# Performance work log

Hardware: AMD Instinct MI355X
Metric: run time of the kernel (lower is better)

The kernel has to match this reference:

```python
import jax, jax.numpy as jnp
import numpy as np

B, T, I, H, F1, C = 512, 128, 128, 768, 256, 10


def setup_inputs() -> dict:
    key = jax.random.key(0)
    ks = jax.random.split(key, 9)
    s = 1.0 / np.sqrt(H).astype(np.float32)  # torch GRUCell/Linear-style scale
    return {
        "x": jax.random.normal(ks[0], (B, T, I), dtype=jnp.float32),
        "w_ih": jax.random.uniform(ks[1], (3 * H, I), jnp.float32, -s, s),
        "w_hh": jax.random.uniform(ks[2], (3 * H, H), jnp.float32, -s, s),
        "b_ih": jax.random.uniform(ks[3], (3 * H,), jnp.float32, -s, s),
        "b_hh": jax.random.uniform(ks[4], (3 * H,), jnp.float32, -s, s),
        "w_fc1": jax.random.uniform(ks[5], (F1, H), jnp.float32, -s, s),
        "b_fc1": jax.random.uniform(ks[6], (F1,), jnp.float32, -s, s),
        "w_fc2": jax.random.uniform(ks[7], (C, F1), jnp.float32, -s, s),
        "b_fc2": jax.random.uniform(ks[8], (C,), jnp.float32, -s, s),
    }


def reference(x, w_ih, w_hh, b_ih, b_hh, w_fc1, b_fc1, w_fc2, b_fc2):
    # x: [B, T, I]. Input projection for all timesteps in one GEMM (same math
    # as per-step GRUCell, since gi does not depend on h).
    gi = jnp.einsum("bti,gi->btg", x, w_ih) + b_ih  # [B, T, 3H]
    h0 = jnp.zeros((x.shape[0], w_hh.shape[1]), x.dtype)

    def step(h, gi_t):
        gh = h @ w_hh.T + b_hh  # [B, 3H]
        i_r, i_z, i_n = jnp.split(gi_t, 3, axis=-1)
        h_r, h_z, h_n = jnp.split(gh, 3, axis=-1)
        r = jax.nn.sigmoid(i_r + h_r)
        z = jax.nn.sigmoid(i_z + h_z)
        n = jnp.tanh(i_n + r * h_n)
        h_new = (1.0 - z) * n + z * h
        return h_new, None

    h, _ = jax.lax.scan(step, h0, jnp.swapaxes(gi, 0, 1))  # scan over T
    out = jax.nn.relu(h @ w_fc1.T + b_fc1)
    logits = out @ w_fc2.T + b_fc2
    return logits
```

## Files before the change

kernel.cpp:

```cpp
#include <hip/hip_runtime.h>
#include <hip/hip_bf16.h>


typedef unsigned short u16;
typedef float    f32x4    __attribute__((ext_vector_type(4)));
typedef unsigned uint32x4 __attribute__((ext_vector_type(4)));
typedef __bf16   bf16x8   __attribute__((ext_vector_type(8)));

#define MFMA16 __builtin_amdgcn_mfma_f32_16x16x32_bf16

#define GLOAD16(gp, lp)                                                        \
  __builtin_amdgcn_global_load_lds(                                            \
      (const __attribute__((address_space(1))) void*)(gp),                     \
      (__attribute__((address_space(3))) void*)(lp), 16, 0, 0)
#define GLOAD16C(gp, lp)                                                       \
  __builtin_amdgcn_global_load_lds(                                            \
      (const __attribute__((address_space(1))) void*)(gp),                     \
      (__attribute__((address_space(3))) void*)(lp), 16, 0, 1)

__device__ __forceinline__ float bf2f(u16 u) {
  unsigned v = ((unsigned)u) << 16;
  return __builtin_bit_cast(float, v);
}
__device__ __forceinline__ u16 f2bf(float f) {
  unsigned x = __builtin_bit_cast(unsigned, f);
  unsigned r = (x + 0x7fffu + ((x >> 16) & 1u)) >> 16;
  return (u16)r;
}
__device__ __forceinline__ float sigm(float x) {
  x = fminf(fmaxf(x, -30.f), 30.f);
  return 1.f / (1.f + __expf(-x));
}
__device__ __forceinline__ float tanhx(float x) {
  x = fminf(fmaxf(x, -15.f), 15.f);
  float ex = __expf(2.f * x);
  return (ex - 1.f) / (ex + 1.f);
}

__global__ __launch_bounds__(256) void k_prep_w(
    const float* __restrict__ w_ih, const float* __restrict__ w_hh,
    u16* __restrict__ Wg) {
  int idx = blockIdx.x * 256 + threadIdx.x;
  int e = idx & 7, c8 = (idx >> 3) & 7;
  int r3 = idx >> 6;
  int r = r3 % 72;
  int jbt = r3 / 72;
  int bt = jbt % 14, jb = jbt / 14;
  int kc = c8 ^ (r & 7);
  int k = bt * 64 + kc * 8 + e;
  int g = r / 24, c = r % 24;
  int grow = g * 768 + jb * 24 + c;
  float v = (k < 768) ? w_hh[grow * 768 + k] : w_ih[grow * 128 + (k - 768)];
  Wg[idx] = f2bf(v);
}

__global__ __launch_bounds__(256) void k_prep_x(
    const float* __restrict__ x, u16* __restrict__ xpk) {
  int idx = blockIdx.x * 256 + threadIdx.x;
  int e = idx & 7, c16 = (idx >> 3) & 15;
  int row = (idx >> 7) & 511;
  int tb = idx >> 16;
  int bt = tb & 1, t = tb >> 1;
  int lc = c16 ^ (row & 15);
  int hl = lc >> 3, kc = lc & 7;
  int i = bt * 64 + kc * 8 + e;
  float v = x[(row * 128 + t) * 128 + i];
  u16 h = f2bf(v);
  xpk[idx] = hl ? f2bf(v - bf2f(h)) : h;
}

__global__ __launch_bounds__(256) void k_prep_fc1t(
    const float* __restrict__ w_fc1, float* __restrict__ wT) {
  int idx = blockIdx.x * 256 + threadIdx.x;
  int k = idx >> 8, n = idx & 255;
  wT[idx] = w_fc1[n * 768 + k];
}

__global__ __launch_bounds__(512) void k_gru_all(
    const u16* __restrict__ Wg, const u16* __restrict__ xpk,
    u16* __restrict__ hA, u16* __restrict__ hB,
    const float* __restrict__ b_ih, const float* __restrict__ b_hh,
    unsigned* __restrict__ bar, unsigned* __restrict__ ctl) {
  __shared__ __align__(16) u16 sW[64512];
  __shared__ __align__(16) u16 sA[2][8192];
  __shared__ unsigned s_asn;
  const int tid = threadIdx.x;
  const int lane = tid & 63, wv = tid >> 6;
  const int mg = wv & 3, sg = wv >> 2;
  const int l15 = lane & 15, lg = lane >> 4;

  if (tid == 0) {
    unsigned xcd;
    asm volatile("s_getreg_b32 %0, hwreg(HW_REG_XCC_ID, 0, 32)" : "=s"(xcd));
    xcd &= 7u;
    unsigned slot = __hip_atomic_fetch_add(&ctl[xcd * 32], 1u,
        __ATOMIC_RELAXED, __HIP_MEMORY_SCOPE_AGENT);
    __hip_atomic_fetch_add(&ctl[256], 1u, __ATOMIC_RELEASE,
                           __HIP_MEMORY_SCOPE_AGENT);
    while (__hip_atomic_load(&ctl[256], __ATOMIC_RELAXED,
                             __HIP_MEMORY_SCOPE_AGENT) < 256u)
      __builtin_amdgcn_s_sleep(8);
    __builtin_amdgcn_fence(__ATOMIC_ACQUIRE, "agent");
    bool ok = (slot < 32u);
    for (int xx = 0; xx < 8; ++xx)
      ok &= (__hip_atomic_load(&ctl[xx * 32], __ATOMIC_RELAXED,
                               __HIP_MEMORY_SCOPE_AGENT) == 32u);
    unsigned bgv, jbv, fen;
    if (ok) { bgv = xcd; jbv = slot; fen = 0u; }
    else    { bgv = (unsigned)blockIdx.x >> 5;
              jbv = (unsigned)blockIdx.x & 31u; fen = 1u; }
    s_asn = bgv | (jbv << 3) | (fen << 8);
  }
  __syncthreads();
  const unsigned asn = s_asn;
  const int bg = asn & 7, jb = (asn >> 3) & 31;
  const bool fence = (asn >> 8) & 1;
  const int mbase = bg * 64;

  {
    const u16* wbase = Wg + (size_t)jb * 64512;
    for (int ch = wv; ch < 126; ch += 8)
      GLOAD16(wbase + ch * 512 + lane * 8, &sW[ch * 512]);
  }
  asm volatile("s_waitcnt vmcnt(0)" ::: "memory");
  __syncthreads();

  const int cc = sg * 16 + l15;
  const int ccv = (cc < 24) ? cc : (cc - 8);
  int aOff[2][2], bOff[3][2];
#pragma unroll
  for (int kk = 0; kk < 2; ++kk) {
    const int sw = (((kk << 2) + lg) ^ (l15 & 7)) << 3;
#pragma unroll
    for (int hl = 0; hl < 2; ++hl)
      aOff[kk][hl] = (mg * 16 + l15) * 128 +
                     ((((hl << 3) + (kk << 2) + lg) ^ l15) << 3);
#pragma unroll
    for (int g = 0; g < 3; ++g)
      bOff[g][kk] = (g * 24 + ccv) * 64 + sw;
  }
  const int schunk = wv * 2;

  const int j = jb * 24 + cc;
  const bool jvalid = (cc < 24);
  float br = 0.f, bz = 0.f, bni = 0.f, bnh = 0.f;
  if (jvalid) {
    br = b_ih[j] + b_hh[j];
    bz = b_ih[768 + j] + b_hh[768 + j];
    bni = b_ih[1536 + j]; bnh = b_hh[1536 + j];
  }
  const int ebt = j >> 6, ekr = j & 63;
  const int ekc = ekr >> 3, eke = ekr & 7;
  unsigned* mybar = bar + bg * 32;

#pragma unroll 1
  for (int t = 0; t < 128; ++t) {
    const u16* hcur = (t & 1) ? hB : hA;
    u16* hnxt = (t & 1) ? hA : hB;
    const u16* xpt = xpk + (size_t)t * 131072;
    const u16* hsl = hcur + mbase * 128;
    const u16* xsl = xpt + mbase * 128;

    f32x4 acc0 = {0.f, 0.f, 0.f, 0.f};
    f32x4 acc1 = {0.f, 0.f, 0.f, 0.f};
    f32x4 acc2 = {0.f, 0.f, 0.f, 0.f};
    f32x4 acc3 = {0.f, 0.f, 0.f, 0.f};

    GLOAD16C(hsl + schunk * 512 + lane * 8, &sA[0][schunk * 512]);
    GLOAD16C(hsl + (schunk + 1) * 512 + lane * 8, &sA[0][(schunk + 1) * 512]);
    asm volatile("s_waitcnt vmcnt(0)" ::: "memory");
    __builtin_amdgcn_s_barrier();
    asm volatile("" ::: "memory");

#pragma unroll
    for (int bt = 0; bt < 14; ++bt) {
      const int buf = bt & 1;
      if (bt < 13) {
        const int nt = bt + 1;
        if (nt < 12) {
          const u16* ab = hsl + nt * 65536;
          GLOAD16C(ab + schunk * 512 + lane * 8, &sA[buf ^ 1][schunk * 512]);
          GLOAD16C(ab + (schunk + 1) * 512 + lane * 8,
                   &sA[buf ^ 1][(schunk + 1) * 512]);
        } else {
          const u16* ab = xsl + (nt - 12) * 65536;
          GLOAD16(ab + schunk * 512 + lane * 8, &sA[buf ^ 1][schunk * 512]);
          GLOAD16(ab + (schunk + 1) * 512 + lane * 8,
                  &sA[buf ^ 1][(schunk + 1) * 512]);
        }
      }
      bf16x8 Ah[2], Al[2], Bf[3][2];
#pragma unroll
      for (int kk = 0; kk < 2; ++kk) {
        Ah[kk] = *(const bf16x8*)&sA[buf][aOff[kk][0]];
        Al[kk] = *(const bf16x8*)&sA[buf][aOff[kk][1]];
#pragma unroll
        for (int g = 0; g < 3; ++g)
          Bf[g][kk] = *(const bf16x8*)&sW[bt * 4608 + bOff[g][kk]];
      }
      __builtin_amdgcn_s_setprio(1);
#pragma unroll
      for (int kk = 0; kk < 2; ++kk)
#pragma unroll
        for (int ps = 0; ps < 2; ++ps) {
          const bf16x8 Aop = ps ? Al[kk] : Ah[kk];
          acc0 = MFMA16(Aop, Bf[0][kk], acc0, 0, 0, 0);
          acc1 = MFMA16(Aop, Bf[1][kk], acc1, 0, 0, 0);
          if (bt < 12) acc2 = MFMA16(Aop, Bf[2][kk], acc2, 0, 0, 0);
          else         acc3 = MFMA16(Aop, Bf[2][kk], acc3, 0, 0, 0);
        }
      __builtin_amdgcn_s_setprio(0);
      if (bt < 13) {
        asm volatile("s_waitcnt vmcnt(0)" ::: "memory");
        __builtin_amdgcn_s_barrier();
        asm volatile("" ::: "memory");
      }
    }

    if (jvalid) {
#pragma unroll
      for (int e = 0; e < 4; ++e) {
        const int row = mbase + mg * 16 + lg * 4 + e;
        const int hidx = (ebt * 512 + row) * 128 + ((ekc ^ (row & 15)) << 3) + eke;
        const float hold = bf2f(hcur[hidx]) + bf2f(hcur[hidx ^ 64]);
        const float rg = sigm(acc0[e] + br);
        const float zg = sigm(acc1[e] + bz);
        const float ng = tanhx(acc3[e] + bni + rg * (acc2[e] + bnh));
        const float hv = (1.f - zg) * ng + zg * hold;
        const u16 uh = f2bf(hv);
        hnxt[hidx] = uh;
        hnxt[hidx ^ 64] = f2bf(hv - bf2f(uh));
      }
    }

    if (t == 127) break;

    __syncthreads();
    if (fence) __builtin_amdgcn_fence(__ATOMIC_RELEASE, "agent");
    if (tid == 0) {
      __hip_atomic_fetch_add(mybar, 1u, __ATOMIC_RELAXED,
                             __HIP_MEMORY_SCOPE_AGENT);
      const unsigned tgt = 32u * (unsigned)(t + 1);
      while (__hip_atomic_load(mybar, __ATOMIC_RELAXED,
                               __HIP_MEMORY_SCOPE_AGENT) < tgt)
        __builtin_amdgcn_s_sleep(2);
    }
    __syncthreads();
    if (fence) __builtin_amdgcn_fence(__ATOMIC_ACQUIRE, "agent");
  }
}

__global__ __launch_bounds__(256) void k_fc1(
    const u16* __restrict__ h, const float* __restrict__ wT,
    const float* __restrict__ b1, float* __restrict__ out) {
  __shared__ float a_s[4][768];
  const int tid = threadIdx.x, rb = blockIdx.x * 4;
#pragma unroll
  for (int r = 0; r < 4; ++r) {
    const int row = rb + r, r16 = row & 15;
    for (int k = tid; k < 768; k += 256) {
      const int bt = k >> 6, kr = k & 63;
      const int idx = (bt * 512 + row) * 128 + (((kr >> 3) ^ r16) << 3) + (kr & 7);
      a_s[r][k] = bf2f(h[idx]) + bf2f(h[idx ^ 64]);
    }
  }
  __syncthreads();
  const int n = tid;
  float ac0 = b1[n], ac1 = ac0, ac2 = ac0, ac3 = ac0;
  for (int k0 = 0; k0 < 768; k0 += 8) {
    float w[8];
#pragma unroll
    for (int u = 0; u < 8; ++u) w[u] = wT[(k0 + u) * 256 + n];
#pragma unroll
    for (int u = 0; u < 8; ++u) {
      ac0 += a_s[0][k0 + u] * w[u];
      ac1 += a_s[1][k0 + u] * w[u];
      ac2 += a_s[2][k0 + u] * w[u];
      ac3 += a_s[3][k0 + u] * w[u];
    }
  }
  out[(rb + 0) * 256 + n] = fmaxf(ac0, 0.f);
  out[(rb + 1) * 256 + n] = fmaxf(ac1, 0.f);
  out[(rb + 2) * 256 + n] = fmaxf(ac2, 0.f);
  out[(rb + 3) * 256 + n] = fmaxf(ac3, 0.f);
}

__global__ __launch_bounds__(256) void k_fc2(
    const float* __restrict__ a, const float* __restrict__ w_fc2,
    const float* __restrict__ b_fc2, float* __restrict__ out) {
  const int lane = threadIdx.x & 63, w = threadIdx.x >> 6;
  const int b = blockIdx.x * 4 + w;
  const f32x4 av = ((const f32x4*)(a + b * 256))[lane];
#pragma unroll
  for (int c = 0; c < 10; ++c) {
    const f32x4 wv = ((const f32x4*)(w_fc2 + c * 256))[lane];
    float s = av[0] * wv[0] + av[1] * wv[1] + av[2] * wv[2] + av[3] * wv[3];
#pragma unroll
    for (int off = 32; off > 0; off >>= 1) s += __shfl_xor(s, off);
    if (lane == 0) out[b * 10 + c] = s + b_fc2[c];
  }
}

extern "C" void kernel_launch(void* const* d_in, const int* in_sizes, int n_in,
                              void* d_out, int out_size, void* d_ws, size_t ws_size,
                              hipStream_t stream) {
  const float* x     = (const float*)d_in[0];
  const float* w_ih  = (const float*)d_in[1];
  const float* w_hh  = (const float*)d_in[2];
  const float* b_ih  = (const float*)d_in[3];
  const float* b_hh  = (const float*)d_in[4];
  const float* w_fc1 = (const float*)d_in[5];
  const float* b_fc1 = (const float*)d_in[6];
  const float* w_fc2 = (const float*)d_in[7];
  const float* b_fc2 = (const float*)d_in[8];
  float* out = (float*)d_out;

  char* ws = (char*)d_ws;
  size_t off = 0;
  auto carve = [&](size_t bytes) {
    char* p = ws + off;
    off += (bytes + 255) & ~(size_t)255;
    return p;
  };
  u16*      Wg   = (u16*)carve(2064384ull * 2);
  u16*      xpk  = (u16*)carve(16777216ull * 2);
  u16*      hpkA = (u16*)carve(786432ull * 2);
  u16*      hpkB = (u16*)carve(786432ull * 2);
  float*    fc1T = (float*)carve(768ull * 256 * 4);
  float*    fc1o = (float*)carve(512ull * 256 * 4);
  unsigned* bar  = (unsigned*)carve(4096);
  unsigned* ctl  = (unsigned*)carve(4096);
  if (off > ws_size) return;

  k_prep_w<<<dim3(8064), dim3(256), 0, stream>>>(w_ih, w_hh, Wg);
  k_prep_x<<<dim3(65536), dim3(256), 0, stream>>>(x, xpk);
  k_prep_fc1t<<<dim3(768), dim3(256), 0, stream>>>(w_fc1, fc1T);
  hipMemsetAsync(hpkA, 0, 786432ull * 2, stream);
  hipMemsetAsync(bar, 0, 4096, stream);
  hipMemsetAsync(ctl, 0, 4096, stream);

  void* kargs[] = {(void*)&Wg, (void*)&xpk, (void*)&hpkA, (void*)&hpkB,
                   (void*)&b_ih, (void*)&b_hh, (void*)&bar, (void*)&ctl};
  hipLaunchCooperativeKernel((const void*)k_gru_all, dim3(256), dim3(512),
                             kargs, 0, stream);

  k_fc1<<<dim3(128), dim3(256), 0, stream>>>(hpkA, fc1T, b_fc1, fc1o);
  k_fc2<<<dim3(128), dim3(256), 0, stream>>>(fc1o, w_fc2, b_fc2, out);
}
```

Measured before the change: 1.280 ms.

## Prefetch next-step x tiles during grid barrier and triple-buffer h loads

The per-step K loop is reordered so the two input-projection (x) K-blocks come first. They are prefetched into LDS while the grid-wide barrier spin of the previous timestep runs, which takes x loads off the critical path after the barrier. Their weights are held in registers, shrinking the LDS weight array, and the h tiles use a triple buffer with partial vmcnt waits so loads can run two blocks ahead. Sigmoid and tanh divisions become hardware reciprocals, trading a little precision for fewer instructions, and the added wait-count logic raises the risk of ordering mistakes.

Measured after the change: 1.105 ms. -13.7%, faster.

```diff
diff --git a/kernel.cpp b/kernel.cpp
--- a/kernel.cpp
+++ b/kernel.cpp
@@ -29,12 +29,12 @@
 }
 __device__ __forceinline__ float sigm(float x) {
   x = fminf(fmaxf(x, -30.f), 30.f);
-  return 1.f / (1.f + __expf(-x));
+  return __builtin_amdgcn_rcpf(1.f + __expf(-x));
 }
 __device__ __forceinline__ float tanhx(float x) {
   x = fminf(fmaxf(x, -15.f), 15.f);
   float ex = __expf(2.f * x);
-  return (ex - 1.f) / (ex + 1.f);
+  return (ex - 1.f) * __builtin_amdgcn_rcpf(ex + 1.f);
 }
 
 __global__ __launch_bounds__(256) void k_prep_w(
@@ -81,8 +81,8 @@
     u16* __restrict__ hA, u16* __restrict__ hB,
     const float* __restrict__ b_ih, const float* __restrict__ b_hh,
     unsigned* __restrict__ bar, unsigned* __restrict__ ctl) {
-  __shared__ __align__(16) u16 sW[64512];
-  __shared__ __align__(16) u16 sA[2][8192];
+  __shared__ __align__(16) u16 sW[55296];
+  __shared__ __align__(16) u16 sA[3][8192];
   __shared__ unsigned s_asn;
   const int tid = threadIdx.x;
   const int lane = tid & 63, wv = tid >> 6;
@@ -117,14 +117,6 @@
   const bool fence = (asn >> 8) & 1;
   const int mbase = bg * 64;
 
-  {
-    const u16* wbase = Wg + (size_t)jb * 64512;
-    for (int ch = wv; ch < 126; ch += 8)
-      GLOAD16(wbase + ch * 512 + lane * 8, &sW[ch * 512]);
-  }
-  asm volatile("s_waitcnt vmcnt(0)" ::: "memory");
-  __syncthreads();
-
   const int cc = sg * 16 + l15;
   const int ccv = (cc < 24) ? cc : (cc - 8);
   int aOff[2][2], bOff[3][2];
@@ -140,6 +132,21 @@
       bOff[g][kk] = (g * 24 + ccv) * 64 + sw;
   }
   const int schunk = wv * 2;
+
+  const u16* wbase = Wg + (size_t)jb * 64512;
+  for (int ch = wv; ch < 108; ch += 8)
+    GLOAD16(wbase + ch * 512 + lane * 8, &sW[ch * 512]);
+  bf16x8 Bx[2][3][2];
+#pragma unroll
+  for (int xb = 0; xb < 2; ++xb)
+#pragma unroll
+    for (int g = 0; g < 3; ++g)
+#pragma unroll
+      for (int kk = 0; kk < 2; ++kk)
+        Bx[xb][g][kk] = __builtin_bit_cast(bf16x8,
+            *(const uint32x4*)(wbase + (12 + xb) * 4608 + bOff[g][kk]));
+  asm volatile("s_waitcnt vmcnt(0)" ::: "memory");
+  __syncthreads();
 
   const int j = jb * 24 + cc;
   const bool jvalid = (cc < 24);
@@ -153,67 +160,76 @@
   const int ekc = ekr >> 3, eke = ekr & 7;
   unsigned* mybar = bar + bg * 32;
 
+  {
+    const u16* xn = xpk + (size_t)mbase * 128;
+    GLOAD16(xn + schunk * 512 + lane * 8, &sA[0][schunk * 512]);
+    GLOAD16(xn + (schunk + 1) * 512 + lane * 8, &sA[0][(schunk + 1) * 512]);
+    GLOAD16(xn + 65536 + schunk * 512 + lane * 8, &sA[1][schunk * 512]);
+    GLOAD16(xn + 65536 + (schunk + 1) * 512 + lane * 8,
+            &sA[1][(schunk + 1) * 512]);
+  }
+
 #pragma unroll 1
   for (int t = 0; t < 128; ++t) {
     const u16* hcur = (t & 1) ? hB : hA;
     u16* hnxt = (t & 1) ? hA : hB;
-    const u16* xpt = xpk + (size_t)t * 131072;
     const u16* hsl = hcur + mbase * 128;
-    const u16* xsl = xpt + mbase * 128;
 
     f32x4 acc0 = {0.f, 0.f, 0.f, 0.f};
     f32x4 acc1 = {0.f, 0.f, 0.f, 0.f};
     f32x4 acc2 = {0.f, 0.f, 0.f, 0.f};
     f32x4 acc3 = {0.f, 0.f, 0.f, 0.f};
 
-    GLOAD16C(hsl + schunk * 512 + lane * 8, &sA[0][schunk * 512]);
-    GLOAD16C(hsl + (schunk + 1) * 512 + lane * 8, &sA[0][(schunk + 1) * 512]);
-    asm volatile("s_waitcnt vmcnt(0)" ::: "memory");
-    __builtin_amdgcn_s_barrier();
-    asm volatile("" ::: "memory");
-
-#pragma unroll
-    for (int bt = 0; bt < 14; ++bt) {
-      const int buf = bt & 1;
-      if (bt < 13) {
-        const int nt = bt + 1;
-        if (nt < 12) {
-          const u16* ab = hsl + nt * 65536;
-          GLOAD16C(ab + schunk * 512 + lane * 8, &sA[buf ^ 1][schunk * 512]);
-          GLOAD16C(ab + (schunk + 1) * 512 + lane * 8,
-                   &sA[buf ^ 1][(schunk + 1) * 512]);
-        } else {
-          const u16* ab = xsl + (nt - 12) * 65536;
-          GLOAD16(ab + schunk * 512 + lane * 8, &sA[buf ^ 1][schunk * 512]);
-          GLOAD16(ab + (schunk + 1) * 512 + lane * 8,
-                  &sA[buf ^ 1][(schunk + 1) * 512]);
-        }
+#pragma unroll
+    for (int b = 0; b < 14; ++b) {
+      if (b < 13) asm volatile("s_waitcnt vmcnt(2)" ::: "memory");
+      else        asm volatile("s_waitcnt vmcnt(0)" ::: "memory");
+      __builtin_amdgcn_s_barrier();
+      asm volatile("" ::: "memory");
+      if (b + 2 < 14) {
+        const u16* ab = hsl + b * 65536;
+        const int nbuf = (b + 2) % 3;
+        GLOAD16C(ab + schunk * 512 + lane * 8, &sA[nbuf][schunk * 512]);
+        GLOAD16C(ab + (schunk + 1) * 512 + lane * 8,
+                 &sA[nbuf][(schunk + 1) * 512]);
       }
-      bf16x8 Ah[2], Al[2], Bf[3][2];
+      const int buf = b % 3;
+      bf16x8 Ah[2], Al[2];
 #pragma unroll
       for (int kk = 0; kk < 2; ++kk) {
         Ah[kk] = *(const bf16x8*)&sA[buf][aOff[kk][0]];
         Al[kk] = *(const bf16x8*)&sA[buf][aOff[kk][1]];
-#pragma unroll
-        for (int g = 0; g < 3; ++g)
-          Bf[g][kk] = *(const bf16x8*)&sW[bt * 4608 + bOff[g][kk]];
       }
-      __builtin_amdgcn_s_setprio(1);
-#pragma unroll
-      for (int kk = 0; kk < 2; ++kk)
-#pragma unroll
-        for (int ps = 0; ps < 2; ++ps) {
-          const bf16x8 Aop = ps ? Al[kk] : Ah[kk];
-          acc0 = MFMA16(Aop, Bf[0][kk], acc0, 0, 0, 0);
-          acc1 = MFMA16(Aop, Bf[1][kk], acc1, 0, 0, 0);
-          if (bt < 12) acc2 = MFMA16(Aop, Bf[2][kk], acc2, 0, 0, 0);
-          else         acc3 = MFMA16(Aop, Bf[2][kk], acc3, 0, 0, 0);
-        }
-      __builtin_amdgcn_s_setprio(0);
-      if (bt < 13) {
-        asm volatile("s_waitcnt vmcnt(0)" ::: "memory");
-        __builtin_amdgcn_s_barrier();
-        asm volatile("" ::: "memory");
+      if (b < 2) {
+        __builtin_amdgcn_s_setprio(1);
+#pragma unroll
+        for (int kk = 0; kk < 2; ++kk)
+#pragma unroll
+          for (int ps = 0; ps < 2; ++ps) {
+            const bf16x8 Aop = ps ? Al[kk] : Ah[kk];
+            acc0 = MFMA16(Aop, Bx[b][0][kk], acc0, 0, 0, 0);
+            acc1 = MFMA16(Aop, Bx[b][1][kk], acc1, 0, 0, 0);
+            acc3 = MFMA16(Aop, Bx[b][2][kk], acc3, 0, 0, 0);
+          }
+        __builtin_amdgcn_s_setprio(0);
+      } else {
+        bf16x8 Bf[3][2];
+#pragma unroll
+        for (int kk = 0; kk < 2; ++kk)
+#pragma unroll
+          for (int g = 0; g < 3; ++g)
+            Bf[g][kk] = *(const bf16x8*)&sW[(b - 2) * 4608 + bOff[g][kk]];
+        __builtin_amdgcn_s_setprio(1);
+#pragma unroll
+        for (int kk = 0; kk < 2; ++kk)
+#pragma unroll
+          for (int ps = 0; ps < 2; ++ps) {
+            const bf16x8 Aop = ps ? Al[kk] : Ah[kk];
+            acc0 = MFMA16(Aop, Bf[0][kk], acc0, 0, 0, 0);
+            acc1 = MFMA16(Aop, Bf[1][kk], acc1, 0, 0, 0);
+            acc2 = MFMA16(Aop, Bf[2][kk], acc2, 0, 0, 0);
+          }
+        __builtin_amdgcn_s_setprio(0);
       }
     }
 
@@ -235,8 +251,16 @@
 
     if (t == 127) break;
 
-    __syncthreads();
+    const u16* xn = xpk + (size_t)(t + 1) * 131072 + mbase * 128;
+    GLOAD16(xn + schunk * 512 + lane * 8, &sA[0][schunk * 512]);
+    asm volatile("s_waitcnt vmcnt(2)" ::: "memory");
     if (fence) __builtin_amdgcn_fence(__ATOMIC_RELEASE, "agent");
+    __builtin_amdgcn_s_barrier();
+    asm volatile("" ::: "memory");
+    GLOAD16(xn + 65536 + schunk * 512 + lane * 8, &sA[1][schunk * 512]);
+    GLOAD16(xn + 65536 + (schunk + 1) * 512 + lane * 8,
+            &sA[1][(schunk + 1) * 512]);
+    GLOAD16(xn + (schunk + 1) * 512 + lane * 8, &sA[0][(schunk + 1) * 512]);
     if (tid == 0) {
       __hip_atomic_fetch_add(mybar, 1u, __ATOMIC_RELAXED,
                              __HIP_MEMORY_SCOPE_AGENT);
@@ -245,8 +269,11 @@
                                __HIP_MEMORY_SCOPE_AGENT) < tgt)
         __builtin_amdgcn_s_sleep(2);
     }
-    __syncthreads();
+    __builtin_amdgcn_s_barrier();
+    asm volatile("" ::: "memory");
     if (fence) __builtin_amdgcn_fence(__ATOMIC_ACQUIRE, "agent");
+    if (wv == 0)
+      asm volatile("s_waitcnt vmcnt(0)" ::: "memory");
   }
 }
 
```
